# Optimization experiments

Hardware: AMD Instinct MI355X
Metric: run time of the kernel (lower is better)

The kernel has to match this reference:

```python
import jax, jax.numpy as jnp
import numpy as np

B, C, E, H = 8, 2048, 1024, 128


def setup_inputs() -> dict:
    key = jax.random.key(0)
    k1, k2, k3, k4 = jax.random.split(key, 4)
    x = jax.random.normal(k1, (B, C, E), dtype=jnp.float32)
    # store projection weights as (E, H) so projection is x @ W
    Wq = jax.random.normal(k2, (E, H), dtype=jnp.float32) * (E ** -0.5)
    Wk = jax.random.normal(k3, (E, H), dtype=jnp.float32) * (E ** -0.5)
    Wv = jax.random.normal(k4, (E, H), dtype=jnp.float32) * (E ** -0.5)
    return {"x": x, "Wq": Wq, "Wk": Wk, "Wv": Wv}


def reference(x, Wq, Wk, Wv):
    # x: (B, C, E) -> out: (B, C, H)
    _, c, e = x.shape
    q = x @ Wq  # (B, C, H)
    k = x @ Wk  # (B, C, H)
    v = x @ Wv  # (B, C, H)
    # NOTE: original scales by embed_size**0.5, not head_size**0.5
    scale = jnp.asarray(e, x.dtype) ** 0.5
    w = jnp.einsum('bqh,bkh->bqk', q, k) / scale  # (B, C, C)
    causal = jnp.tril(jnp.ones((c, c), dtype=bool))
    w = jnp.where(causal, w, -jnp.inf)
    w = jax.nn.softmax(w, axis=-1)
    # dropout_rate = 0.0 -> identity (eval mode)
    out = w @ v  # (B, C, H)
    return out
```

## Files before the change

### kernel.cpp

```cpp
#include <hip/hip_runtime.h>
#include <hip/hip_bf16.h>
#include <stdint.h>

#define B_ 8
#define C_ 2048
#define E_ 1024
#define H_ 128
#define M_ (B_*C_)
#define SLOTS_B 144

typedef __attribute__((ext_vector_type(8))) short bf16x8;
typedef __attribute__((ext_vector_type(4))) float f32x4;

__device__ __forceinline__ unsigned short f2bf(float f) {
    union { float f; unsigned int u; } v; v.f = f;
    unsigned int u = v.u;
    u += 0x7fff + ((u >> 16) & 1);
    return (unsigned short)(u >> 16);
}
__device__ __forceinline__ float bf2f(unsigned short u) {
    union { unsigned int i; float f; } v; v.i = ((unsigned int)u) << 16; return v.f;
}

#define GLOAD_LDS16(g, l) \
    __builtin_amdgcn_global_load_lds((const __attribute__((address_space(1))) void*)(g), \
                                     (__attribute__((address_space(3))) void*)(l), 16, 0, 0)

__global__ __launch_bounds__(256) void wt2_kernel(const float* __restrict__ Wq,
                                                  const float* __restrict__ Wk,
                                                  const float* __restrict__ Wv,
                                                  unsigned short* __restrict__ WT2) {
    int z = blockIdx.y;
    const float* W = (z == 0) ? Wq : (z == 1) ? Wk : Wv;
    unsigned short* o = WT2 + (size_t)z * H_ * E_;
    int gid = blockIdx.x * 256 + threadIdx.x;
    int g = gid >> 7, h = gid & 127;
    unsigned short t[8];
#pragma unroll
    for (int j = 0; j < 8; ++j)
        t[j] = f2bf(W[(size_t)(g * 8 + j) * H_ + h]);
    *(bf16x8*)&o[(size_t)(g * 128 + h) * 8] = *(const bf16x8*)t;
}

__global__ __launch_bounds__(256) void proj_kernel(const float* __restrict__ x,
                                                   const unsigned short* __restrict__ WT2,
                                                   unsigned short* __restrict__ QKV) {
    __shared__ __align__(16) unsigned short As[2][64][64];

    const int tid = threadIdx.x;
    const int wid = tid >> 6, lane = tid & 63;
    const int lrow = lane & 15, lq = lane >> 4;
    const int wr = wid >> 1, wc = wid & 1;
    const int row0 = blockIdx.x * 64;
    const int w = blockIdx.y;
    const unsigned short* wt = WT2 + (size_t)w * H_ * E_;

    const int arow = tid >> 2;
    const int ag0 = (tid & 3) * 2;
    const float* xrow = x + (size_t)(row0 + arow) * E_ + ag0 * 8;

    f32x4 acc[2][4];
#pragma unroll
    for (int mi = 0; mi < 2; ++mi)
#pragma unroll
        for (int ni = 0; ni < 4; ++ni) acc[mi][ni] = (f32x4){0.f, 0.f, 0.f, 0.f};

    float4 a0, a1, a2, a3;
    bf16x8 breg[2][8];

    auto A_LOAD = [&](int t) {
        const float* xs = xrow + t * 64;
        a0 = *(const float4*)xs;       a1 = *(const float4*)(xs + 4);
        a2 = *(const float4*)(xs + 8); a3 = *(const float4*)(xs + 12);
    };
    auto A_WRITE = [&](int buf) {
        unsigned short t0[8] = {f2bf(a0.x), f2bf(a0.y), f2bf(a0.z), f2bf(a0.w),
                                f2bf(a1.x), f2bf(a1.y), f2bf(a1.z), f2bf(a1.w)};
        unsigned short t1[8] = {f2bf(a2.x), f2bf(a2.y), f2bf(a2.z), f2bf(a2.w),
                                f2bf(a3.x), f2bf(a3.y), f2bf(a3.z), f2bf(a3.w)};
        *(bf16x8*)&As[buf][arow][(ag0 ^ (arow & 7)) * 8]       = *(const bf16x8*)t0;
        *(bf16x8*)&As[buf][arow][((ag0 + 1) ^ (arow & 7)) * 8] = *(const bf16x8*)t1;
    };

    A_LOAD(0);
#pragma unroll
    for (int i = 0; i < 8; ++i) {
        int g = (i >> 2) * 4 + lq;
        int rb = wc * 64 + (i & 3) * 16 + lrow;
        breg[0][i] = *(const bf16x8*)&wt[(size_t)(g * 128 + rb) * 8];
    }
    A_WRITE(0);

#pragma unroll
    for (int t = 0; t < 16; ++t) {
        const int cur = t & 1;
        __syncthreads();
        if (t < 15) {
            A_LOAD(t + 1);
#pragma unroll
            for (int i = 0; i < 8; ++i) {
                int g = (t + 1) * 8 + (i >> 2) * 4 + lq;
                int rb = wc * 64 + (i & 3) * 16 + lrow;
                breg[cur ^ 1][i] = *(const bf16x8*)&wt[(size_t)(g * 128 + rb) * 8];
            }
        }
#pragma unroll
        for (int ks = 0; ks < 2; ++ks) {
            const int g = ks * 4 + lq;
            bf16x8 af[2];
#pragma unroll
            for (int mi = 0; mi < 2; ++mi) {
                int ra = wr * 32 + mi * 16 + lrow;
                af[mi] = *(const bf16x8*)&As[cur][ra][(g ^ (ra & 7)) * 8];
            }
#pragma unroll
            for (int mi = 0; mi < 2; ++mi)
#pragma unroll
                for (int ni = 0; ni < 4; ++ni)
                    acc[mi][ni] = __builtin_amdgcn_mfma_f32_16x16x32_bf16(
                        af[mi], breg[cur][ks * 4 + ni], acc[mi][ni], 0, 0, 0);
        }
        if (t < 15) A_WRITE(cur ^ 1);
    }

    if (w < 2) {
        const float qs = (w == 0) ? 0.03125f : 1.0f;
        unsigned short* outp = QKV + (size_t)w * M_ * H_;
#pragma unroll
        for (int mi = 0; mi < 2; ++mi) {
            int r0 = row0 + wr * 32 + mi * 16 + lq * 4;
#pragma unroll
            for (int ni = 0; ni < 4; ++ni) {
                int col = wc * 64 + ni * 16 + lrow;
#pragma unroll
                for (int r = 0; r < 4; ++r)
                    outp[(size_t)(r0 + r) * H_ + col] = f2bf(acc[mi][ni][r] * qs);
            }
        }
    } else {
        unsigned short* vt = QKV + (size_t)2 * M_ * H_;
        int b = row0 / C_;
        int cbase = row0 % C_;
#pragma unroll
        for (int mi = 0; mi < 2; ++mi) {
            int c0 = cbase + wr * 32 + mi * 16 + lq * 4;
#pragma unroll
            for (int ni = 0; ni < 4; ++ni) {
                int h = wc * 64 + ni * 16 + lrow;
                __align__(8) unsigned short p[4] = {f2bf(acc[mi][ni][0]), f2bf(acc[mi][ni][1]),
                                                    f2bf(acc[mi][ni][2]), f2bf(acc[mi][ni][3])};
                *(uint2*)&vt[((size_t)b * H_ + h) * C_ + c0] = *(const uint2*)p;
            }
        }
    }
}

__global__ __launch_bounds__(256) void attn_kernel(const unsigned short* __restrict__ QKV,
                                                   unsigned short* __restrict__ PO,
                                                   float* __restrict__ ML,
                                                   float* __restrict__ out) {
    __shared__ __align__(16) unsigned short Ks[2][64][128];
    __shared__ __align__(16) unsigned short Vt[2][128][64];
    __shared__ __align__(16) unsigned short Ps[4][16][72];

    const unsigned short* Q  = QKV;
    const unsigned short* K  = QKV + (size_t)M_ * H_;
    const unsigned short* VT = QKV + (size_t)2 * M_ * H_;

    const int tid = threadIdx.x, wid = tid >> 6, lane = tid & 63;
    const int lrow = lane & 15, lq = lane >> 4, lk = lq * 8;
    const int rr = blockIdx.x;
    const int b = blockIdx.y;

    int j = 0;
#pragma unroll
    for (int jj = 1; jj < 32; ++jj) {
        int q = jj >> 2, s = jj & 3;
        if (jj + 2 * q * (q - 1) + s * q <= rr) j = jj;
    }
    const int qj = j >> 2, sj = j & 3;
    const int Cj = j + 2 * qj * (qj - 1) + sj * qj;
    const int c = rr - Cj;
    const int nch = qj + 1;
    const int t0 = c * 4;
    const int t1 = min(t0 + 4, j + 1);

    const int q0w = j * 64 + wid * 16;
    const unsigned short* Kb  = K  + (size_t)b * C_ * H_;
    const unsigned short* VTb = VT + (size_t)b * H_ * C_;
    const int qrow0 = q0w + lq * 4;

    const int krow = tid >> 4, kg = tid & 15;
    const int vrow = tid >> 3, vg = tid & 7;

    bf16x8 qf[4];
#pragma unroll
    for (int kf = 0; kf < 4; ++kf)
        qf[kf] = *(const bf16x8*)&Q[((size_t)b * C_ + q0w + lrow) * H_ + kf * 32 + lk];

    f32x4 o[8];
#pragma unroll
    for (int nf = 0; nf < 8; ++nf) o[nf] = (f32x4){0.f, 0.f, 0.f, 0.f};
    float m[4] = {-INFINITY, -INFINITY, -INFINITY, -INFINITY};
    float l[4] = {0.f, 0.f, 0.f, 0.f};

    auto STAGE = [&](int buf, int t) {
        const int kv0 = t * 64;
#pragma unroll
        for (int s = 0; s < 4; ++s) {
            int r = s * 16 + krow;
            GLOAD_LDS16(&Kb[(size_t)(kv0 + r) * H_ + ((kg ^ (r & 15)) * 8)],
                        (char*)&Ks[buf][0][0] + s * 4096 + tid * 16);
        }
#pragma unroll
        for (int s = 0; s < 4; ++s) {
            int h = s * 32 + vrow;
            GLOAD_LDS16(&VTb[(size_t)h * C_ + kv0 + ((vg ^ (h & 7)) * 8)],
                        (char*)&Vt[buf][0][0] + s * 4096 + tid * 16);
        }
    };

    STAGE(0, t0);

    for (int t = t0; t < t1; ++t) {
        const int cur = (t - t0) & 1;
        __syncthreads();
        if (t + 1 < t1) STAGE(cur ^ 1, t + 1);

        const int kv0 = t * 64;
        f32x4 s[4];
#pragma unroll
        for (int nf = 0; nf < 4; ++nf) {
            s[nf] = (f32x4){0.f, 0.f, 0.f, 0.f};
            const int rk = nf * 16 + lrow;
#pragma unroll
            for (int kf = 0; kf < 4; ++kf) {
                bf16x8 kb = *(const bf16x8*)&Ks[cur][rk][((kf * 4 + lq) ^ (rk & 15)) * 8];
                s[nf] = __builtin_amdgcn_mfma_f32_16x16x32_bf16(qf[kf], kb, s[nf], 0, 0, 0);
            }
        }
        bf16x8 vb[8][2];
#pragma unroll
        for (int nf = 0; nf < 8; ++nf) {
            const int h = nf * 16 + lrow;
#pragma unroll
            for (int kf2 = 0; kf2 < 2; ++kf2)
                vb[nf][kf2] = *(const bf16x8*)&Vt[cur][h][((kf2 * 4 + lq) ^ (h & 7)) * 8];
        }

        if (t == j) {
#pragma unroll
            for (int nf = 0; nf < 4; ++nf) {
                int key = kv0 + nf * 16 + lrow;
#pragma unroll
                for (int r = 0; r < 4; ++r)
                    if (key > qrow0 + r) s[nf][r] = -INFINITY;
            }
        }
        float mt[4] = {-INFINITY, -INFINITY, -INFINITY, -INFINITY};
#pragma unroll
        for (int nf = 0; nf < 4; ++nf)
#pragma unroll
            for (int r = 0; r < 4; ++r) mt[r] = fmaxf(mt[r], s[nf][r]);
#pragma unroll
        for (int r = 0; r < 4; ++r)
#pragma unroll
            for (int off = 1; off < 16; off <<= 1)
                mt[r] = fmaxf(mt[r], __shfl_xor(mt[r], off));

        float corr[4];
#pragma unroll
        for (int r = 0; r < 4; ++r) {
            float mn = fmaxf(m[r], mt[r]);
            corr[r] = __expf(m[r] - mn);
            m[r] = mn;
        }
        float ps[4] = {0.f, 0.f, 0.f, 0.f};
#pragma unroll
        for (int nf = 0; nf < 4; ++nf)
#pragma unroll
            for (int r = 0; r < 4; ++r) {
                float p = __expf(s[nf][r] - m[r]);
                ps[r] += p;
                Ps[wid][lq * 4 + r][nf * 16 + lrow] = f2bf(p);
            }
#pragma unroll
        for (int r = 0; r < 4; ++r) {
#pragma unroll
            for (int off = 1; off < 16; off <<= 1) ps[r] += __shfl_xor(ps[r], off);
            l[r] = l[r] * corr[r] + ps[r];
        }
#pragma unroll
        for (int nf = 0; nf < 8; ++nf)
#pragma unroll
            for (int r = 0; r < 4; ++r) o[nf][r] *= corr[r];

        bf16x8 pa[2];
#pragma unroll
        for (int kf2 = 0; kf2 < 2; ++kf2)
            pa[kf2] = *(const bf16x8*)&Ps[wid][lrow][kf2 * 32 + lk];
#pragma unroll
        for (int nf = 0; nf < 8; ++nf)
#pragma unroll
            for (int kf2 = 0; kf2 < 2; ++kf2)
                o[nf] = __builtin_amdgcn_mfma_f32_16x16x32_bf16(pa[kf2], vb[nf][kf2], o[nf], 0, 0, 0);
    }

    if (nch == 1) {
#pragma unroll
        for (int nf = 0; nf < 8; ++nf) {
            int col = nf * 16 + lrow;
#pragma unroll
            for (int r = 0; r < 4; ++r)
                out[((size_t)b * C_ + qrow0 + r) * H_ + col] = o[nf][r] / l[r];
        }
    } else {
        const int slot = b * SLOTS_B + rr;
        unsigned short* po = PO + (size_t)slot * 64 * 128;
        const int rl0 = wid * 16 + lq * 4;
#pragma unroll
        for (int nf = 0; nf < 8; ++nf) {
            int col = nf * 16 + lrow;
#pragma unroll
            for (int r = 0; r < 4; ++r)
                po[(size_t)(rl0 + r) * 128 + col] = f2bf(o[nf][r]);
        }
        if (lrow == 0) {
            float* ml = ML + (size_t)slot * 128;
#pragma unroll
            for (int r = 0; r < 4; ++r) {
                ml[rl0 + r] = m[r];
                ml[64 + rl0 + r] = l[r];
            }
        }
    }
}

__global__ __launch_bounds__(256) void combine_kernel(const unsigned short* __restrict__ PO,
                                                      const float* __restrict__ ML,
                                                      float* __restrict__ out) {
    const int j = blockIdx.x + 4;
    const int b = blockIdx.y;
    const int q = j >> 2, s = j & 3;
    const int Cj = j + 2 * q * (q - 1) + s * q;
    const int nch = q + 1;
    const int base = b * SLOTS_B + Cj;
    const int row = threadIdx.x >> 2;
    const int colg = (threadIdx.x & 3) * 32;

    float mstar = -INFINITY;
    for (int c = 0; c < nch; ++c)
        mstar = fmaxf(mstar, ML[(size_t)(base + c) * 128 + row]);

    float denom = 0.f;
    float acc[32];
#pragma unroll
    for (int i = 0; i < 32; ++i) acc[i] = 0.f;

    for (int c = 0; c < nch; ++c) {
        float mc = ML[(size_t)(base + c) * 128 + row];
        float lc = ML[(size_t)(base + c) * 128 + 64 + row];
        float w = __expf(mc - mstar);
        denom += w * lc;
        const unsigned short* p = PO + (size_t)(base + c) * 64 * 128 + (size_t)row * 128 + colg;
#pragma unroll
        for (int k = 0; k < 4; ++k) {
            bf16x8 v = *(const bf16x8*)&p[k * 8];
#pragma unroll
            for (int e = 0; e < 8; ++e)
                acc[k * 8 + e] += w * bf2f(((unsigned short*)&v)[e]);
        }
    }
    float inv = 1.f / denom;
    float* op = out + ((size_t)b * C_ + j * 64 + row) * H_ + colg;
#pragma unroll
    for (int k = 0; k < 8; ++k) {
        float4 st = {acc[k * 4] * inv, acc[k * 4 + 1] * inv, acc[k * 4 + 2] * inv, acc[k * 4 + 3] * inv};
        *(float4*)&op[k * 4] = st;
    }
}

extern "C" void kernel_launch(void* const* d_in, const int* in_sizes, int n_in,
                              void* d_out, int out_size, void* d_ws, size_t ws_size,
                              hipStream_t stream) {
    const float* x  = (const float*)d_in[0];
    const float* Wq = (const float*)d_in[1];
    const float* Wk = (const float*)d_in[2];
    const float* Wv = (const float*)d_in[3];
    float* out = (float*)d_out;

    unsigned short* WT2 = (unsigned short*)d_ws;
    unsigned short* QKV = WT2 + (size_t)3 * H_ * E_;
    unsigned short* PO  = QKV + (size_t)3 * M_ * H_;
    float*          ML  = (float*)(PO + (size_t)8 * SLOTS_B * 64 * 128);

    wt2_kernel<<<dim3(E_ / 8 * H_ / 256, 3), 256, 0, stream>>>(Wq, Wk, Wv, WT2);
    proj_kernel<<<dim3(M_ / 64, 3), 256, 0, stream>>>(x, WT2, QKV);
    attn_kernel<<<dim3(SLOTS_B, B_), 256, 0, stream>>>(QKV, PO, ML, out);
    combine_kernel<<<dim3(28, B_), 256, 0, stream>>>(PO, ML, out);
}
```

Baseline: 84.89 us.

## Deepen projection GEMM prefetch pipeline to two stages ahead with named registers

Rewrites the projection kernel's main loop as a fully unrolled macro sequence. Global loads of x tiles run up to three steps ahead and weight fragments two steps ahead, held in two named register sets instead of indexed arrays. The goal is to hide global memory latency behind the MFMA work and to stop the compiler from spilling indexed arrays. In exchange, more live registers raise register pressure and could lower occupancy.

```diff
diff --git a/kernel.cpp b/kernel.cpp
--- a/kernel.cpp
+++ b/kernel.cpp
@@ -42,6 +42,54 @@
     *(bf16x8*)&o[(size_t)(g * 128 + h) * 8] = *(const bf16x8*)t;
 }
 
+#define MF(a, b, c) __builtin_amdgcn_mfma_f32_16x16x32_bf16((a), (b), (c), 0, 0, 0)
+
+#define ALOAD(S, T) { const float* xs_ = xrow + (T) * 64; \
+    a##S##_0 = *(const float4*)xs_;        a##S##_1 = *(const float4*)(xs_ + 4); \
+    a##S##_2 = *(const float4*)(xs_ + 8);  a##S##_3 = *(const float4*)(xs_ + 12); }
+
+#define AWRITE(S, BUF) { \
+    unsigned short t0_[8] = {f2bf(a##S##_0.x), f2bf(a##S##_0.y), f2bf(a##S##_0.z), f2bf(a##S##_0.w), \
+                             f2bf(a##S##_1.x), f2bf(a##S##_1.y), f2bf(a##S##_1.z), f2bf(a##S##_1.w)}; \
+    unsigned short t1_[8] = {f2bf(a##S##_2.x), f2bf(a##S##_2.y), f2bf(a##S##_2.z), f2bf(a##S##_2.w), \
+                             f2bf(a##S##_3.x), f2bf(a##S##_3.y), f2bf(a##S##_3.z), f2bf(a##S##_3.w)}; \
+    *(bf16x8*)&As[BUF][arow][(ag0 ^ (arow & 7)) * 8]       = *(const bf16x8*)t0_; \
+    *(bf16x8*)&As[BUF][arow][((ag0 + 1) ^ (arow & 7)) * 8] = *(const bf16x8*)t1_; }
+
+#define BLOAD(S, T) { const unsigned short* wp_ = wbase + (size_t)(T) * 8192; \
+    b##S##0 = *(const bf16x8*)(wp_);        b##S##1 = *(const bf16x8*)(wp_ + 128); \
+    b##S##2 = *(const bf16x8*)(wp_ + 256);  b##S##3 = *(const bf16x8*)(wp_ + 384); \
+    b##S##4 = *(const bf16x8*)(wp_ + 4096); b##S##5 = *(const bf16x8*)(wp_ + 4224); \
+    b##S##6 = *(const bf16x8*)(wp_ + 4352); b##S##7 = *(const bf16x8*)(wp_ + 4480); }
+
+#define COMPUTE(BUF, S) { \
+    bf16x8 af00 = *(const bf16x8*)&As[BUF][ra0][(lq ^ (ra0 & 7)) * 8]; \
+    bf16x8 af01 = *(const bf16x8*)&As[BUF][ra1][(lq ^ (ra1 & 7)) * 8]; \
+    acc[0][0] = MF(af00, b##S##0, acc[0][0]);  acc[1][0] = MF(af01, b##S##0, acc[1][0]); \
+    acc[0][1] = MF(af00, b##S##1, acc[0][1]);  acc[1][1] = MF(af01, b##S##1, acc[1][1]); \
+    acc[0][2] = MF(af00, b##S##2, acc[0][2]);  acc[1][2] = MF(af01, b##S##2, acc[1][2]); \
+    acc[0][3] = MF(af00, b##S##3, acc[0][3]);  acc[1][3] = MF(af01, b##S##3, acc[1][3]); \
+    bf16x8 af10 = *(const bf16x8*)&As[BUF][ra0][((4 + lq) ^ (ra0 & 7)) * 8]; \
+    bf16x8 af11 = *(const bf16x8*)&As[BUF][ra1][((4 + lq) ^ (ra1 & 7)) * 8]; \
+    acc[0][0] = MF(af10, b##S##4, acc[0][0]);  acc[1][0] = MF(af11, b##S##4, acc[1][0]); \
+    acc[0][1] = MF(af10, b##S##5, acc[0][1]);  acc[1][1] = MF(af11, b##S##5, acc[1][1]); \
+    acc[0][2] = MF(af10, b##S##6, acc[0][2]);  acc[1][2] = MF(af11, b##S##6, acc[1][2]); \
+    acc[0][3] = MF(af10, b##S##7, acc[0][3]);  acc[1][3] = MF(af11, b##S##7, acc[1][3]); }
+
+#define EVEN_STEP(K) { \
+    __syncthreads(); \
+    AWRITE(B, 1);                                   \
+    if ((K) + 3 <= 15) ALOAD(B, (K) + 3); \
+    COMPUTE(0, A);                                  \
+    if ((K) + 2 <= 15) BLOAD(A, (K) + 2); }
+
+#define ODD_STEP(K) { \
+    __syncthreads(); \
+    if ((K) + 1 <= 15) AWRITE(A, 0);                \
+    if ((K) + 3 <= 15) ALOAD(A, (K) + 3); \
+    COMPUTE(1, B);                                  \
+    if ((K) + 2 <= 15) BLOAD(B, (K) + 2); }
+
 __global__ __launch_bounds__(256) void proj_kernel(const float* __restrict__ x,
                                                    const unsigned short* __restrict__ WT2,
                                                    unsigned short* __restrict__ QKV) {
@@ -58,6 +106,9 @@
     const int arow = tid >> 2;
     const int ag0 = (tid & 3) * 2;
     const float* xrow = x + (size_t)(row0 + arow) * E_ + ag0 * 8;
+    const int ra0 = wr * 32 + lrow, ra1 = wr * 32 + 16 + lrow;
+
+    const unsigned short* wbase = wt + (size_t)(lq * 128 + wc * 64 + lrow) * 8;
 
     f32x4 acc[2][4];
 #pragma unroll
@@ -65,63 +116,19 @@
 #pragma unroll
         for (int ni = 0; ni < 4; ++ni) acc[mi][ni] = (f32x4){0.f, 0.f, 0.f, 0.f};
 
-    float4 a0, a1, a2, a3;
-    bf16x8 breg[2][8];
-
-    auto A_LOAD = [&](int t) {
-        const float* xs = xrow + t * 64;
-        a0 = *(const float4*)xs;       a1 = *(const float4*)(xs + 4);
-        a2 = *(const float4*)(xs + 8); a3 = *(const float4*)(xs + 12);
-    };
-    auto A_WRITE = [&](int buf) {
-        unsigned short t0[8] = {f2bf(a0.x), f2bf(a0.y), f2bf(a0.z), f2bf(a0.w),
-                                f2bf(a1.x), f2bf(a1.y), f2bf(a1.z), f2bf(a1.w)};
-        unsigned short t1[8] = {f2bf(a2.x), f2bf(a2.y), f2bf(a2.z), f2bf(a2.w),
-                                f2bf(a3.x), f2bf(a3.y), f2bf(a3.z), f2bf(a3.w)};
-        *(bf16x8*)&As[buf][arow][(ag0 ^ (arow & 7)) * 8]       = *(const bf16x8*)t0;
-        *(bf16x8*)&As[buf][arow][((ag0 + 1) ^ (arow & 7)) * 8] = *(const bf16x8*)t1;
-    };
-
-    A_LOAD(0);
-#pragma unroll
-    for (int i = 0; i < 8; ++i) {
-        int g = (i >> 2) * 4 + lq;
-        int rb = wc * 64 + (i & 3) * 16 + lrow;
-        breg[0][i] = *(const bf16x8*)&wt[(size_t)(g * 128 + rb) * 8];
-    }
-    A_WRITE(0);
-
-#pragma unroll
-    for (int t = 0; t < 16; ++t) {
-        const int cur = t & 1;
-        __syncthreads();
-        if (t < 15) {
-            A_LOAD(t + 1);
-#pragma unroll
-            for (int i = 0; i < 8; ++i) {
-                int g = (t + 1) * 8 + (i >> 2) * 4 + lq;
-                int rb = wc * 64 + (i & 3) * 16 + lrow;
-                breg[cur ^ 1][i] = *(const bf16x8*)&wt[(size_t)(g * 128 + rb) * 8];
-            }
-        }
-#pragma unroll
-        for (int ks = 0; ks < 2; ++ks) {
-            const int g = ks * 4 + lq;
-            bf16x8 af[2];
-#pragma unroll
-            for (int mi = 0; mi < 2; ++mi) {
-                int ra = wr * 32 + mi * 16 + lrow;
-                af[mi] = *(const bf16x8*)&As[cur][ra][(g ^ (ra & 7)) * 8];
-            }
-#pragma unroll
-            for (int mi = 0; mi < 2; ++mi)
-#pragma unroll
-                for (int ni = 0; ni < 4; ++ni)
-                    acc[mi][ni] = __builtin_amdgcn_mfma_f32_16x16x32_bf16(
-                        af[mi], breg[cur][ks * 4 + ni], acc[mi][ni], 0, 0, 0);
-        }
-        if (t < 15) A_WRITE(cur ^ 1);
-    }
+    float4 aA_0, aA_1, aA_2, aA_3, aB_0, aB_1, aB_2, aB_3;
+    bf16x8 bA0, bA1, bA2, bA3, bA4, bA5, bA6, bA7;
+    bf16x8 bB0, bB1, bB2, bB3, bB4, bB5, bB6, bB7;
+
+    ALOAD(A, 0); BLOAD(A, 0);
+    ALOAD(B, 1); BLOAD(B, 1);
+    AWRITE(A, 0);
+    ALOAD(A, 2);
+
+    EVEN_STEP(0)  ODD_STEP(1)  EVEN_STEP(2)  ODD_STEP(3)
+    EVEN_STEP(4)  ODD_STEP(5)  EVEN_STEP(6)  ODD_STEP(7)
+    EVEN_STEP(8)  ODD_STEP(9)  EVEN_STEP(10) ODD_STEP(11)
+    EVEN_STEP(12) ODD_STEP(13) EVEN_STEP(14) ODD_STEP(15)
 
     if (w < 2) {
         const float qs = (w == 0) ? 0.03125f : 1.0f;
```

Result: no change. 83.96 us (-1.1%).
